# Kernel tuning notes

Measured on AMD Instinct MI355X. Metric: run time of the kernel, lower is better.

The kernel has to match this reference:

```python
import jax, jax.numpy as jnp
import numpy as np

NUM_GROUPS = 32
EPS = 1e-6


def group_norm(x, gamma, beta):
    # x: (B, C, H, W), 32 groups, eps=1e-6, affine
    B, C, H, W = x.shape
    xg = x.reshape(B, NUM_GROUPS, C // NUM_GROUPS, H, W)
    mean = xg.mean(axis=(2, 3, 4), keepdims=True)
    var = xg.var(axis=(2, 3, 4), keepdims=True)
    xn = ((xg - mean) * jax.lax.rsqrt(var + EPS)).reshape(B, C, H, W)
    return xn * gamma[None, :, None, None] + beta[None, :, None, None]


def conv1x1(x, w, b):
    # 1x1 conv == channel matmul. x: (B,C,H,W), w: (O,C), b: (O,)
    return jnp.einsum('bchw,oc->bohw', x, w) + b[None, :, None, None]


def setup_inputs() -> dict:
    key = jax.random.key(0)
    B, C, H, W = 16, 512, 32, 32
    ks = jax.random.split(key, 12)
    s = 1.0 / np.sqrt(C)
    return {
        'x': jax.random.normal(ks[0], (B, C, H, W), dtype=jnp.float32),
        'gn_gamma': jnp.ones((C,), dtype=jnp.float32),
        'gn_beta': jnp.zeros((C,), dtype=jnp.float32),
        'wq': jax.random.normal(ks[1], (C, C), dtype=jnp.float32) * s,
        'bq': jnp.zeros((C,), dtype=jnp.float32),
        'wk': jax.random.normal(ks[2], (C, C), dtype=jnp.float32) * s,
        'bk': jnp.zeros((C,), dtype=jnp.float32),
        'wv': jax.random.normal(ks[3], (C, C), dtype=jnp.float32) * s,
        'bv': jnp.zeros((C,), dtype=jnp.float32),
        'wp': jax.random.normal(ks[4], (C, C), dtype=jnp.float32) * s,
        'bp': jnp.zeros((C,), dtype=jnp.float32),
    }


def reference(x, gn_gamma, gn_beta, wq, bq, wk, bk, wv, bv, wp, bp):
    B, C, H, W = x.shape
    residual = x
    xn = group_norm(x, gn_gamma, gn_beta)
    q = conv1x1(xn, wq, bq).reshape(B, C, H * W)  # (B, C, HW)
    k = conv1x1(xn, wk, bk).reshape(B, C, H * W)
    v = conv1x1(xn, wv, bv).reshape(B, C, H * W)
    scale = C ** (-0.5)
    # energy[b,i,j] = q_i . k_j
    energy = jnp.einsum('bci,bcj->bij', q, k) * scale
    attn = jax.nn.softmax(energy, axis=-1)
    # out[b,c,i] = sum_j attn[b,i,j] * v[b,c,j]
    out = jnp.einsum('bij,bcj->bci', attn, v).reshape(B, C, H, W)
    out = conv1x1(out, wp, bp)
    return out + residual
```

## Files before the change

### kernel.cpp

```cpp
#include <hip/hip_runtime.h>
#include <hip/hip_bf16.h>

using bf16 = __hip_bfloat16;

typedef __attribute__((ext_vector_type(8))) __bf16 bf16x8;
typedef __attribute__((ext_vector_type(4))) float floatx4;

#define EPS 1e-6f

#define RAW_BARRIER()  asm volatile("s_barrier" ::: "memory")
#define WAIT_VM8()     asm volatile("s_waitcnt vmcnt(8)" ::: "memory")
#define WAIT_VM4()     asm volatile("s_waitcnt vmcnt(4)" ::: "memory")
#define WAIT_VM0()     asm volatile("s_waitcnt vmcnt(0)" ::: "memory")
#define SCHED_FENCE()  __builtin_amdgcn_sched_barrier(0)
#define PRIO1()        __builtin_amdgcn_s_setprio(1)
#define PRIO0()        __builtin_amdgcn_s_setprio(0)

__device__ __forceinline__ void load_lds16(const void* g, void* l) {
    __builtin_amdgcn_global_load_lds(
        (const __attribute__((address_space(1))) void*)g,
        (__attribute__((address_space(3))) void*)l, 16, 0, 0);
}

__device__ __forceinline__ void storeOut(float* p, float v) { *p = v; }
__device__ __forceinline__ void storeOut(bf16* p, float v) { *p = __float2bfloat16(v); }

#define MFMA16(a, b, c) __builtin_amdgcn_mfma_f32_16x16x32_bf16(a, b, c, 0, 0, 0)

template <int BIAS_MODE, int RESID_EN, int QKV, typename OutT>
__global__ __launch_bounds__(256, 2) void gemm2b(
    const bf16* __restrict__ A, long long aStride, int lda,
    const bf16* __restrict__ B, long long bStride, int ldb,
    OutT* __restrict__ D, long long dStride, int ldd,
    bf16* __restrict__ vout, long long vStride,
    const float* __restrict__ bias,
    const float* __restrict__ resid, long long rStride, int ldr,
    int K, int tpb, int gx)
{
    constexpr int HB = 8192;
    extern __shared__ char smem[];

    const unsigned chunk = gridDim.x >> 3;
    const unsigned glob  = (blockIdx.x & 7) * chunk + (blockIdx.x >> 3);
    const unsigned z  = glob / (unsigned)tpb;
    const unsigned t  = glob % (unsigned)tpb;
    const int m0 = (int)(t / (unsigned)gx) << 7;
    const int n0 = (int)(t % (unsigned)gx) << 7;

    const int tid  = threadIdx.x;
    const int lane = tid & 63;
    const int wave = tid >> 6;
    const int wm   = wave >> 1;
    const int wn   = wave & 1;

    const bf16* Ab = A + (size_t)z * aStride + (size_t)m0 * lda;
    const bf16* Bb = B + (size_t)z * bStride + (size_t)n0 * ldb;

    floatx4 acc[4][4];
#pragma unroll
    for (int i = 0; i < 4; ++i)
#pragma unroll
        for (int j = 0; j < 4; ++j) acc[i][j] = (floatx4){0.f, 0.f, 0.f, 0.f};

    const int laneRow = lane & 15;
    const int laneKq  = lane >> 4;
    const int kqs16   = (laneKq ^ ((laneRow >> 1) & 3)) << 4;
    const int arow0   = wm * 64 + laneRow;
    const int brow0   = wn * 64 + laneRow;

    auto stage = [&](int kt, int h) {
        char* Adst = smem + ((kt & 1) * 2 + h) * HB;
        char* Bdst = smem + 4 * HB + ((kt & 1) * 2 + h) * HB;
        const int kb = (kt << 6) + (h << 5);
#pragma unroll
        for (int u = 0; u < 2; ++u) {
            const int idx = tid + u * 256;
            const int r  = idx >> 2;
            const int qs = (idx & 3) ^ ((idx >> 3) & 3);
            load_lds16(Ab + (size_t)r * lda + kb + qs * 8, Adst + idx * 16);
        }
#pragma unroll
        for (int u = 0; u < 2; ++u) {
            const int idx = tid + u * 256;
            const int r  = idx >> 2;
            const int qs = (idx & 3) ^ ((idx >> 3) & 3);
            load_lds16(Bb + (size_t)r * ldb + kb + qs * 8, Bdst + idx * 16);
        }
    };

    const int nt = K >> 6;
    stage(0, 0); stage(0, 1); stage(1, 0);

    for (int kt = 0; kt < nt; ++kt) {
        const char* Ablk = smem + (kt & 1) * 2 * HB;
        const char* Bblk = smem + 4 * HB + (kt & 1) * 2 * HB;
        const bool lastT = (kt == nt - 1);

        if (lastT) WAIT_VM4(); else WAIT_VM8();
        RAW_BARRIER();
        bf16x8 af[4], bfr[4];
#pragma unroll
        for (int im = 0; im < 4; ++im)
            af[im] = *(const bf16x8*)(Ablk + (arow0 + im * 16) * 64 + kqs16);
#pragma unroll
        for (int in = 0; in < 4; ++in)
            bfr[in] = *(const bf16x8*)(Bblk + (brow0 + in * 16) * 64 + kqs16);
        if (kt + 1 < nt) stage(kt + 1, 1);
        RAW_BARRIER();
        PRIO1();
#pragma unroll
        for (int im = 0; im < 4; ++im)
#pragma unroll
            for (int in = 0; in < 4; ++in)
                acc[im][in] = MFMA16(af[im], bfr[in], acc[im][in]);
        PRIO0();

        if (lastT) WAIT_VM0(); else WAIT_VM8();
        RAW_BARRIER();
#pragma unroll
        for (int im = 0; im < 4; ++im)
            af[im] = *(const bf16x8*)(Ablk + HB + (arow0 + im * 16) * 64 + kqs16);
#pragma unroll
        for (int in = 0; in < 4; ++in)
            bfr[in] = *(const bf16x8*)(Bblk + HB + (brow0 + in * 16) * 64 + kqs16);
        if (kt + 2 < nt) stage(kt + 2, 0);
        RAW_BARRIER();
        PRIO1();
#pragma unroll
        for (int im = 0; im < 4; ++im)
#pragma unroll
            for (int in = 0; in < 4; ++in)
                acc[im][in] = MFMA16(af[im], bfr[in], acc[im][in]);
        PRIO0();
    }

    const size_t dbase = (size_t)z * dStride;
#pragma unroll
    for (int im = 0; im < 4; ++im) {
        const int gmb = m0 + wm * 64 + im * 16 + (laneKq << 2);
#pragma unroll
        for (int in = 0; in < 4; ++in) {
            const int gn = n0 + wn * 64 + in * 16 + laneRow;
            float bn = 0.f;
            if (BIAS_MODE == 2) bn = bias[gn];
            if (QKV && n0 >= 1024) {
                union { bf16 h[4]; ushort4 u; } pk;
#pragma unroll
                for (int r = 0; r < 4; ++r)
                    pk.h[r] = __float2bfloat16(acc[im][in][r] + bn);
                *(ushort4*)(vout + (size_t)z * vStride +
                            (size_t)(gn - 1024) * 1024 + gmb) = pk.u;
            } else {
#pragma unroll
                for (int r = 0; r < 4; ++r) {
                    const int gm = gmb + r;
                    float v = acc[im][in][r];
                    if (BIAS_MODE == 1) v += bias[gm];
                    if (BIAS_MODE == 2) v += bn;
                    if (RESID_EN)
                        v += resid[(size_t)z * rStride + (size_t)gm * ldr + gn];
                    storeOut(D + dbase + (size_t)gm * ldd + gn, v);
                }
            }
        }
    }
}

__global__ __launch_bounds__(512, 2) void fattn(
    const bf16* __restrict__ qkT,
    const bf16* __restrict__ vv,
    bf16* __restrict__ O2,
    float scale)
{
    constexpr int KT = 32768;
    extern __shared__ char smem[];
    __shared__ __align__(16) char plds[4 * 1024];
    __shared__ float rsLDS[2][64];

    const int bid  = blockIdx.x;
    const int glob = (bid & 7) * 32 + (bid >> 3);
    const int b    = glob >> 4;
    const int i0   = (glob & 15) << 6;

    const int tid     = threadIdx.x;
    const int lane    = tid & 63;
    const int wave    = tid >> 6;
    const int jh      = wave & 1;
    const int ih      = wave >> 1;
    const int laneRow = lane & 15;
    const int laneKq  = lane >> 4;
    const int kqs16   = (laneKq ^ ((laneRow >> 1) & 3)) << 4;
    const int sw2     = ((laneRow >> 1) & 3) << 1;

    const bf16* Qb = qkT + (size_t)b * 1048576 +
                     (size_t)(i0 + ih * 16 + laneRow) * 1024;
    const bf16* Kb = qkT + (size_t)b * 1048576 + 512;
    const bf16* Vb = vv + (size_t)b * 524288;

    bf16x8 qf[16];
#pragma unroll
    for (int ks = 0; ks < 16; ++ks)
        qf[ks] = *(const bf16x8*)(Qb + ks * 32 + laneKq * 8);

    floatx4 acc[4][4];
#pragma unroll
    for (int mf = 0; mf < 4; ++mf)
#pragma unroll
        for (int ni = 0; ni < 4; ++ni) acc[mf][ni] = (floatx4){0.f, 0.f, 0.f, 0.f};
    float rs = 0.f;

    auto stageK = [&](int jt) {
        char* dst = smem + (jt & 1) * KT;
        const bf16* src = Kb + ((size_t)jt << 5) * 1024;
#pragma unroll
        for (int u = 0; u < 4; ++u) {
            const int idx = tid + u * 512;
            const int kk = idx >> 7;
            const int j  = (idx >> 2) & 31;
            const int p  = idx & 3;
            load_lds16(src + (size_t)j * 1024 + kk * 32 + 8 * (p ^ ((j >> 1) & 3)),
                       dst + idx * 16);
        }
    };
    auto stageV = [&](int jt) {
        char* dst = smem + 2 * KT + (jt & 1) * KT;
        const bf16* src = Vb + (jt << 5);
#pragma unroll
        for (int u = 0; u < 4; ++u) {
            const int idx = tid + u * 512;
            const int c = idx >> 2;
            const int p = idx & 3;
            load_lds16(src + (size_t)c * 1024 + 8 * (p ^ ((c >> 1) & 3)),
                       dst + idx * 16);
        }
    };

    stageK(0); stageV(0); stageK(1); stageV(1);

    for (int jt = 0; jt < 32; ++jt) {
        if (jt == 31) WAIT_VM0(); else WAIT_VM8();
        RAW_BARRIER();
        const char* Kt = smem + (jt & 1) * KT;
        const char* Vt = smem + 2 * KT + (jt & 1) * KT;

        floatx4 s = (floatx4){0.f, 0.f, 0.f, 0.f};
#pragma unroll
        for (int ks = 0; ks < 16; ++ks) {
            bf16x8 kf = *(const bf16x8*)(Kt + ks * 2048 +
                                         (jh * 16 + laneRow) * 64 + kqs16);
            s = MFMA16(kf, qf[ks], s);
        }

        union { bf16 h[4]; unsigned long long u; } w;
#pragma unroll
        for (int r = 0; r < 4; ++r) {
            float v = __expf(s[r] * scale);
            rs += v;
            w.h[r] = __float2bfloat16(v);
        }
        *(unsigned long long*)(plds + ih * 1024 + laneRow * 64 +
                               ((4 * jh + laneKq) ^ sw2) * 8) = w.u;
        asm volatile("s_waitcnt lgkmcnt(0)" ::: "memory");
        RAW_BARRIER();
        SCHED_FENCE();
        bf16x8 pf[4];
#pragma unroll
        for (int ni = 0; ni < 4; ++ni)
            pf[ni] = *(const bf16x8*)(plds + ni * 1024 + laneRow * 64 + kqs16);

        PRIO1();
#pragma unroll
        for (int mf = 0; mf < 4; ++mf) {
            bf16x8 vf = *(const bf16x8*)(Vt +
                (wave * 64 + mf * 16 + laneRow) * 64 + kqs16);
#pragma unroll
            for (int ni = 0; ni < 4; ++ni)
                acc[mf][ni] = MFMA16(vf, pf[ni], acc[mf][ni]);
        }
        PRIO0();

        RAW_BARRIER();
        if (jt + 2 < 32) { stageK(jt + 2); stageV(jt + 2); }
    }

    rs += __shfl_xor(rs, 16);
    rs += __shfl_xor(rs, 32);
    if (lane < 16) rsLDS[jh][ih * 16 + lane] = rs;
    __syncthreads();

#pragma unroll
    for (int ni = 0; ni < 4; ++ni) {
        const int row = ni * 16 + laneRow;
        const float ri = 1.f / (rsLDS[0][row] + rsLDS[1][row]);
        bf16* Ob = O2 + (size_t)b * 524288 +
                   (size_t)(i0 + row) * 512 + wave * 64 + (laneKq << 2);
#pragma unroll
        for (int mf = 0; mf < 4; ++mf) {
            union { bf16 h[4]; ushort4 u; } pk;
#pragma unroll
            for (int r = 0; r < 4; ++r)
                pk.h[r] = __float2bfloat16(acc[mf][ni][r] * ri);
            *(ushort4*)(Ob + mf * 16) = pk.u;
        }
    }
}

__global__ __launch_bounds__(256) void gn_stats(const float* __restrict__ x,
                                                float* __restrict__ stats)
{
    const int bg = blockIdx.x;
    const float4* p = (const float4*)(x + (size_t)bg * 16384);
    float s = 0.f, ss = 0.f;
    for (int i = threadIdx.x; i < 4096; i += 256) {
        float4 v = p[i];
        s  += v.x + v.y + v.z + v.w;
        ss += v.x * v.x + v.y * v.y + v.z * v.z + v.w * v.w;
    }
#pragma unroll
    for (int off = 32; off; off >>= 1) {
        s  += __shfl_down(s, off);
        ss += __shfl_down(ss, off);
    }
    __shared__ float rsm[4], rss[4];
    const int wv = threadIdx.x >> 6;
    if ((threadIdx.x & 63) == 0) { rsm[wv] = s; rss[wv] = ss; }
    __syncthreads();
    if (threadIdx.x == 0) {
        float S  = rsm[0] + rsm[1] + rsm[2] + rsm[3];
        float SS = rss[0] + rss[1] + rss[2] + rss[3];
        float mean = S * (1.f / 16384.f);
        float var  = SS * (1.f / 16384.f) - mean * mean;
        stats[2 * bg]     = mean;
        stats[2 * bg + 1] = rsqrtf(var + EPS);
    }
}

__global__ __launch_bounds__(256) void gn_apply_t(const float* __restrict__ x,
                                                  const float* __restrict__ stats,
                                                  const float* __restrict__ gamma,
                                                  const float* __restrict__ beta,
                                                  bf16* __restrict__ xnT)
{
    __shared__ bf16 tile[32][36];
    const int b = blockIdx.z, c0 = blockIdx.y * 32, i0 = blockIdx.x * 32;
    {
        const int cc = threadIdx.x >> 3;
        const int i4 = (threadIdx.x & 7) << 2;
        const int c  = c0 + cc;
        const float mean = stats[2 * ((b << 5) + (c >> 4))];
        const float rstd = stats[2 * ((b << 5) + (c >> 4)) + 1];
        const float a  = gamma[c] * rstd;
        const float bb = beta[c] - mean * a;
        float4 v = *(const float4*)(x + (((size_t)(b * 512 + c)) << 10) + i0 + i4);
        tile[cc][i4 + 0] = __float2bfloat16(v.x * a + bb);
        tile[cc][i4 + 1] = __float2bfloat16(v.y * a + bb);
        tile[cc][i4 + 2] = __float2bfloat16(v.z * a + bb);
        tile[cc][i4 + 3] = __float2bfloat16(v.w * a + bb);
    }
    __syncthreads();
    {
        const int ii = threadIdx.x >> 3;
        const int c4 = (threadIdx.x & 7) << 2;
        union { bf16 h[4]; uint2 u; } pk;
        pk.h[0] = tile[c4 + 0][ii];
        pk.h[1] = tile[c4 + 1][ii];
        pk.h[2] = tile[c4 + 2][ii];
        pk.h[3] = tile[c4 + 3][ii];
        *((uint2*)(xnT + (((size_t)(b * 1024 + i0 + ii)) << 9) + c0 + c4)) = pk.u;
    }
}

__global__ __launch_bounds__(256) void prep(
    const float* __restrict__ wq, const float* __restrict__ wk,
    const float* __restrict__ wv, const float* __restrict__ wp,
    bf16* __restrict__ wqkvb, bf16* __restrict__ wpb,
    const float* __restrict__ bq, const float* __restrict__ bk,
    const float* __restrict__ bv, float* __restrict__ bqkv)
{
    const int id = blockIdx.x;
    if (id < 1024) {
        const int w = id >> 8;
        const float* src = (w == 0) ? wq : (w == 1) ? wk : (w == 2) ? wv : wp;
        bf16* dst = (w < 3) ? (wqkvb + (size_t)w * 262144) : wpb;
        const int g = (id & 255) * 256 + threadIdx.x;
        float4 v = ((const float4*)src)[g];
        union { bf16 h[4]; uint2 u; } pk;
        pk.h[0] = __float2bfloat16(v.x);
        pk.h[1] = __float2bfloat16(v.y);
        pk.h[2] = __float2bfloat16(v.z);
        pk.h[3] = __float2bfloat16(v.w);
        ((uint2*)dst)[g] = pk.u;
    } else {
        for (int t = threadIdx.x; t < 1536; t += 256)
            bqkv[t] = (t < 512) ? bq[t] : (t < 1024) ? bk[t - 512] : bv[t - 1024];
    }
}

extern "C" void kernel_launch(void* const* d_in, const int* in_sizes, int n_in,
                              void* d_out, int out_size, void* d_ws, size_t ws_size,
                              hipStream_t stream)
{
    const float* x     = (const float*)d_in[0];
    const float* gamma = (const float*)d_in[1];
    const float* beta  = (const float*)d_in[2];
    const float* wq    = (const float*)d_in[3];
    const float* bq    = (const float*)d_in[4];
    const float* wk    = (const float*)d_in[5];
    const float* bk    = (const float*)d_in[6];
    const float* wv    = (const float*)d_in[7];
    const float* bv    = (const float*)d_in[8];
    const float* wp    = (const float*)d_in[9];
    const float* bp    = (const float*)d_in[10];
    float* out = (float*)d_out;

    char* ws = (char*)d_ws;
    size_t off = 0;
    auto alloc = [&](size_t bytes) -> char* {
        char* p = ws + off;
        off += (bytes + 255) & ~(size_t)255;
        return p;
    };

    const long long S  = 1024, C = 512;
    const long long BS = S * C;
    const long long ES = S * S;

    float* stats  = (float*)alloc(512 * 2 * sizeof(float));
    float* bqkv   = (float*)alloc(1536 * sizeof(float));
    bf16* wqkvb = (bf16*)alloc((size_t)3 * C * C * 2);
    bf16* wpb   = (bf16*)alloc((size_t)C * C * 2);
    bf16* xnT   = (bf16*)alloc((size_t)16 * BS * 2);
    bf16* qkT   = (bf16*)alloc((size_t)16 * ES * 2);
    bf16* vv    = (bf16*)alloc((size_t)16 * BS * 2);
    bf16* O2    = (bf16*)alloc((size_t)16 * BS * 2);

    hipFuncSetAttribute((const void*)gemm2b<2, 0, 1, bf16>,
                        hipFuncAttributeMaxDynamicSharedMemorySize, 65536);
    hipFuncSetAttribute((const void*)gemm2b<1, 1, 0, float>,
                        hipFuncAttributeMaxDynamicSharedMemorySize, 65536);
    hipFuncSetAttribute((const void*)fattn,
                        hipFuncAttributeMaxDynamicSharedMemorySize, 131072);

    prep<<<1025, 256, 0, stream>>>(wq, wk, wv, wp, wqkvb, wpb, bq, bk, bv, bqkv);

    gn_stats<<<512, 256, 0, stream>>>(x, stats);
    gn_apply_t<<<dim3(32, 16, 16), 256, 0, stream>>>(x, stats, gamma, beta, xnT);

    gemm2b<2, 0, 1, bf16><<<1536, 256, 65536, stream>>>(
        xnT, BS, 512, wqkvb, 0, 512, qkT, ES, 1024, vv, BS,
        bqkv, nullptr, 0, 0, 512, 96, 12);

    const float scale = 0.044194173824159216f;
    fattn<<<256, 512, 131072, stream>>>(qkT, vv, O2, scale);

    gemm2b<1, 1, 0, float><<<512, 256, 65536, stream>>>(
        wpb, 0, 512, O2, BS, 512, out, BS, 1024, nullptr, 0,
        bp, x, BS, 1024, 512, 32, 8);
}
```

Measured before the change: 227.9 us.

## Load V fragments directly to registers and triple-buffer K in LDS

In the fused attention kernel, V tiles are no longer staged through LDS. Each wave instead loads its own V fragments from global memory straight into registers, one tile ahead. K staging moves to a 3-slot LDS ring, which removes the trailing barrier before the next stage, and the dynamic LDS allocation shrinks from 128KB to 96KB. The aim is to cut LDS traffic and one barrier per iteration, at the cost of extra registers and uncoalesced, unshared direct global reads of V.

```diff
diff --git a/kernel.cpp b/kernel.cpp
--- a/kernel.cpp
+++ b/kernel.cpp
@@ -195,7 +195,8 @@
     const bf16* Qb = qkT + (size_t)b * 1048576 +
                      (size_t)(i0 + ih * 16 + laneRow) * 1024;
     const bf16* Kb = qkT + (size_t)b * 1048576 + 512;
-    const bf16* Vb = vv + (size_t)b * 524288;
+    const bf16* Vb = vv + (size_t)b * 524288 +
+                     (size_t)(wave * 64 + laneRow) * 1024 + laneKq * 8;
 
     bf16x8 qf[16];
 #pragma unroll
@@ -210,7 +211,7 @@
     float rs = 0.f;
 
     auto stageK = [&](int jt) {
-        char* dst = smem + (jt & 1) * KT;
+        char* dst = smem + (jt % 3) * KT;
         const bf16* src = Kb + ((size_t)jt << 5) * 1024;
 #pragma unroll
         for (int u = 0; u < 4; ++u) {
@@ -222,26 +223,25 @@
                        dst + idx * 16);
         }
     };
-    auto stageV = [&](int jt) {
-        char* dst = smem + 2 * KT + (jt & 1) * KT;
-        const bf16* src = Vb + (jt << 5);
-#pragma unroll
-        for (int u = 0; u < 4; ++u) {
-            const int idx = tid + u * 512;
-            const int c = idx >> 2;
-            const int p = idx & 3;
-            load_lds16(src + (size_t)c * 1024 + 8 * (p ^ ((c >> 1) & 3)),
-                       dst + idx * 16);
-        }
+
+    bf16x8 vf[4];
+    auto loadV = [&](int jt) {
+        const bf16* vs = Vb + (jt << 5);
+#pragma unroll
+        for (int mf = 0; mf < 4; ++mf)
+            vf[mf] = *(const bf16x8*)(vs + (size_t)mf * 16384);
     };
 
-    stageK(0); stageV(0); stageK(1); stageV(1);
+    stageK(0);
+    stageK(1);
+    SCHED_FENCE();
+    loadV(0);
+    SCHED_FENCE();
 
     for (int jt = 0; jt < 32; ++jt) {
-        if (jt == 31) WAIT_VM0(); else WAIT_VM8();
-        RAW_BARRIER();
-        const char* Kt = smem + (jt & 1) * KT;
-        const char* Vt = smem + 2 * KT + (jt & 1) * KT;
+        if (jt == 31) WAIT_VM4(); else WAIT_VM8();
+        RAW_BARRIER();
+        const char* Kt = smem + (jt % 3) * KT;
 
         floatx4 s = (floatx4){0.f, 0.f, 0.f, 0.f};
 #pragma unroll
@@ -268,19 +268,20 @@
         for (int ni = 0; ni < 4; ++ni)
             pf[ni] = *(const bf16x8*)(plds + ni * 1024 + laneRow * 64 + kqs16);
 
+        if (jt == 31) WAIT_VM0(); else WAIT_VM4();
+
         PRIO1();
 #pragma unroll
-        for (int mf = 0; mf < 4; ++mf) {
-            bf16x8 vf = *(const bf16x8*)(Vt +
-                (wave * 64 + mf * 16 + laneRow) * 64 + kqs16);
+        for (int mf = 0; mf < 4; ++mf)
 #pragma unroll
             for (int ni = 0; ni < 4; ++ni)
-                acc[mf][ni] = MFMA16(vf, pf[ni], acc[mf][ni]);
-        }
+                acc[mf][ni] = MFMA16(vf[mf], pf[ni], acc[mf][ni]);
         PRIO0();
 
-        RAW_BARRIER();
-        if (jt + 2 < 32) { stageK(jt + 2); stageV(jt + 2); }
+        if (jt + 1 < 32) loadV(jt + 1);
+        SCHED_FENCE();
+        if (jt + 2 < 32) stageK(jt + 2);
+        SCHED_FENCE();
     }
 
     rs += __shfl_xor(rs, 16);
@@ -439,7 +440,7 @@
     hipFuncSetAttribute((const void*)gemm2b<1, 1, 0, float>,
                         hipFuncAttributeMaxDynamicSharedMemorySize, 65536);
     hipFuncSetAttribute((const void*)fattn,
-                        hipFuncAttributeMaxDynamicSharedMemorySize, 131072);
+                        hipFuncAttributeMaxDynamicSharedMemorySize, 98304);
 
     prep<<<1025, 256, 0, stream>>>(wq, wk, wv, wp, wqkvb, wpb, bq, bk, bv, bqkv);
 
@@ -451,7 +452,7 @@
         bqkv, nullptr, 0, 0, 512, 96, 12);
 
     const float scale = 0.044194173824159216f;
-    fattn<<<256, 512, 131072, stream>>>(qkT, vv, O2, scale);
+    fattn<<<256, 512, 98304, stream>>>(qkT, vv, O2, scale);
 
     gemm2b<1, 1, 0, float><<<512, 256, 65536, stream>>>(
         wpb, 0, 512, O2, BS, 512, out, BS, 1024, nullptr, 0,
```

Measured after the change: 240.7 us. 1.06x slower.
